# Performance work log

Measured on AMD Instinct MI355X. Metric: run time of the kernel, lower is better.

## Reference

```python
import jax, jax.numpy as jnp
import numpy as np

NEG_SLOPE = 0.2  # PyG GATv2Conv default negative_slope


def gatv2_layer(x, src, dst, edge_attr, Wl, bl, Wr, br, We, att, bias, n_nodes):
    """Faithful PyG GATv2Conv (concat=True, eval mode / no dropout).
    x: [N, Fin]; src/dst: [E]; edge_attr: [E, Fe]; att: [H, C].
    Returns [N, H*C].
    """
    H, C = att.shape
    xl = (x @ Wl + bl).reshape(-1, H, C)        # source-side transform (x_j)
    xr = (x @ Wr + br).reshape(-1, H, C)        # target-side transform (x_i)
    e_emb = (edge_attr @ We).reshape(-1, H, C)
    # per-edge pre-activation: x_i + x_j + edge
    g = jax.nn.leaky_relu(xl[src] + xr[dst] + e_emb, NEG_SLOPE)  # [E, H, C]
    logits = jnp.einsum('ehc,hc->eh', g, att)                    # [E, H]
    # segment softmax grouped by destination node
    m = jax.ops.segment_max(logits, dst, num_segments=n_nodes)   # [N, H]
    m = jnp.where(jnp.isfinite(m), m, 0.0)                       # empty segments
    a = jnp.exp(logits - m[dst])
    denom = jax.ops.segment_sum(a, dst, num_segments=n_nodes)    # [N, H]
    alpha = a / (denom[dst] + 1e-16)
    msg = xl[src] * alpha[:, :, None]                            # [E, H, C]
    out = jax.ops.segment_sum(msg, dst, num_segments=n_nodes)    # [N, H, C]
    return out.reshape(n_nodes, H * C) + bias


def setup_inputs() -> dict:
    key = jax.random.key(0)
    ks = jax.random.split(key, 24)
    N, E = 100000, 1600000
    Fin, Hd, Fe = 6, 64, 2
    g = lambda k, shp: (jax.random.normal(k, shp, dtype=jnp.float32) * 0.1)
    inp = {
        'x': jax.random.normal(ks[0], (N, Fin), dtype=jnp.float32),
        'edge_index': jax.random.randint(ks[1], (2, E), 0, N, dtype=jnp.int32),
        'edge_attr': jax.random.normal(ks[2], (E, Fe), dtype=jnp.float32),
        # layer 1: heads=2, out=64 -> H*C = 128
        'Wl1': g(ks[3], (Fin, 128)), 'bl1': jnp.zeros((128,), jnp.float32),
        'Wr1': g(ks[4], (Fin, 128)), 'br1': jnp.zeros((128,), jnp.float32),
        'We1': g(ks[5], (Fe, 128)),
        'att1': g(ks[6], (2, Hd)),
        'bias1': jnp.zeros((128,), jnp.float32),
        # layer 2: heads=1, in=128, out=64
        'Wl2': g(ks[7], (128, Hd)), 'bl2': jnp.zeros((Hd,), jnp.float32),
        'Wr2': g(ks[8], (128, Hd)), 'br2': jnp.zeros((Hd,), jnp.float32),
        'We2': g(ks[9], (Fe, Hd)),
        'att2': g(ks[10], (1, Hd)),
        'bias2': jnp.zeros((Hd,), jnp.float32),
        # MLP head
        'Wh1': g(ks[11], (Hd, Hd)), 'bh1': jnp.zeros((Hd,), jnp.float32),
        'Wh2': g(ks[12], (Hd, 1)), 'bh2': jnp.zeros((1,), jnp.float32),
    }
    return inp


def reference(x, edge_index, edge_attr,
              Wl1, bl1, Wr1, br1, We1, att1, bias1,
              Wl2, bl2, Wr2, br2, We2, att2, bias2,
              Wh1, bh1, Wh2, bh2):
    N = x.shape[0]
    src, dst = edge_index[0], edge_index[1]
    h = gatv2_layer(x, src, dst, edge_attr, Wl1, bl1, Wr1, br1, We1, att1, bias1, N)
    h = jax.nn.relu(h)
    h = gatv2_layer(h, src, dst, edge_attr, Wl2, bl2, Wr2, br2, We2, att2, bias2, N)
    h = jax.nn.relu(h)
    out = jax.nn.relu(h @ Wh1 + bh1) @ Wh2 + bh2  # [N, 1]
    return out[:, 0]
```

## Files before the change

### kernel.cpp

```cpp
#include <hip/hip_runtime.h>
#include <hip/hip_bf16.h>

#define NEG_SLOPE 0.2f
#define LOG2E 1.44269504088896f

#define NB_SHIFT 9
#define NB_NODES 512
#define NBLK_PART 256

typedef _Float16 half8 __attribute__((ext_vector_type(8)));
typedef _Float16 half4 __attribute__((ext_vector_type(4)));
typedef _Float16 half2t __attribute__((ext_vector_type(2)));

__device__ __forceinline__ void ld4(float* d, const float* p) {
    float4 t = *(const float4*)p;
    d[0] = t.x; d[1] = t.y; d[2] = t.z; d[3] = t.w;
}

__device__ __forceinline__ unsigned pack2h(float a, float b) {
    union { half2t h; unsigned u; } pk;
    pk.h[0] = (_Float16)a; pk.h[1] = (_Float16)b;
    return pk.u;
}

__device__ __forceinline__ half2t u2h2(unsigned u) {
    union { unsigned u; half2t h; } c; c.u = u; return c.h;
}
__device__ __forceinline__ half2t f2h2(float a, float b) {
    half2t r; r[0] = (_Float16)a; r[1] = (_Float16)b; return r;
}

#if __has_builtin(__builtin_amdgcn_perm)
#define PERMB(a, b, s) __builtin_amdgcn_perm((a), (b), (s))
#else
__device__ __forceinline__ unsigned PERMB(unsigned a, unsigned b, unsigned s) {
    unsigned long long v = ((unsigned long long)a << 32) | b;
    unsigned r = 0;
#pragma unroll
    for (int i = 0; i < 4; ++i) {
        unsigned idx = (s >> (8 * i)) & 0xFF;
        r |= ((unsigned)(v >> (8 * idx)) & 0xFF) << (8 * i);
    }
    return r;
}
#endif

#if __has_builtin(__builtin_amdgcn_fdot2)
#define FDOT2(a, b, c) __builtin_amdgcn_fdot2((a), (b), (c), false)
#else
#define FDOT2(a, b, c) fmaf((float)(a)[1], (float)(b)[1], fmaf((float)(a)[0], (float)(b)[0], (c)))
#endif

#define DPP_ADD(x, ctrl) \
    ((x) + __int_as_float(__builtin_amdgcn_update_dpp(0, __float_as_int(x), (ctrl), 0xf, 0xf, true)))
#define ROW_REDUCE16(x) do { \
    x = DPP_ADD(x, 0x128); \
    x = DPP_ADD(x, 0x124); \
    x = DPP_ADD(x, 0x122); \
    x = DPP_ADD(x, 0x121); \
} while (0)

#define CHGRP(xl2, xr2, wa, wb, at2, ex, ey, logit) do { \
    half2t z_ = (xl2) + (xr2); \
    z_ = __builtin_elementwise_fma((ex), (wa), z_); \
    z_ = __builtin_elementwise_fma((ey), (wb), z_); \
    z_ = __builtin_elementwise_max(z_, z_ * NEGS); \
    logit = FDOT2(z_, (at2), logit); \
} while (0)

__global__ void __launch_bounds__(256) prepA_kernel(
    const float* __restrict__ x,
    const float* __restrict__ Wl1, const float* __restrict__ bl1,
    const float* __restrict__ Wr1, const float* __restrict__ br1,
    _Float16* __restrict__ xlh, _Float16* __restrict__ xrh, int N,
    const int* __restrict__ dstv, int* __restrict__ M, int E, int EPB, int NB)
{
    __shared__ int hist[256];
    int blk = blockIdx.x, t = threadIdx.x;
    bool doA = (blk < NBLK_PART);
    if (doA) {
        if (t < NB) hist[t] = 0;
        __syncthreads();
        int s0 = blk * EPB;
        int s1 = min(s0 + EPB, E);
        for (int e = s0 + t; e < s1; e += 256)
            atomicAdd(&hist[((unsigned)dstv[e]) >> NB_SHIFT], 1);
    }

    int gt = blk * 256 + t;
    int n = gt >> 6, tt = gt & 63;
    if (n < N) {
        int h = tt >> 5;
        int cp = tt & 31;
        int c0 = h * 64 + 2 * cp;
        const float* xrow = x + (size_t)n * 6;
        float la = bl1[c0], lb = bl1[c0 + 1];
        float ra = br1[c0], rb = br1[c0 + 1];
#pragma unroll
        for (int f = 0; f < 6; ++f) {
            float xv = xrow[f];
            la = fmaf(xv, Wl1[f * 128 + c0], la);
            lb = fmaf(xv, Wl1[f * 128 + c0 + 1], lb);
            ra = fmaf(xv, Wr1[f * 128 + c0], ra);
            rb = fmaf(xv, Wr1[f * 128 + c0 + 1], rb);
        }
        int pos = (cp >> 1) * 8 + h * 4 + (cp & 1) * 2;
        *(unsigned*)(xlh + (size_t)n * 128 + pos) = pack2h(la, lb);
        *(unsigned*)(xrh + (size_t)n * 128 + pos) = pack2h(ra, rb);
    }

    if (doA) {
        __syncthreads();
        if (t < NB) M[t * NBLK_PART + blk] = hist[t];
    }
}

__global__ void __launch_bounds__(256) partB1_scanrow(
    int* __restrict__ M, int* __restrict__ btot)
{
    __shared__ int lds[256];
    int bkt = blockIdx.x, t = threadIdx.x;
    int cnt = M[bkt * NBLK_PART + t];
    lds[t] = cnt;
    __syncthreads();
    for (int s = 1; s < 256; s <<= 1) {
        int v = (t >= s) ? lds[t - s] : 0;
        __syncthreads();
        lds[t] += v;
        __syncthreads();
    }
    M[bkt * NBLK_PART + t] = lds[t] - cnt;
    if (t == 255) btot[bkt] = lds[255];
}

__global__ void __launch_bounds__(256) partC_scatter(
    const int* __restrict__ srcv, const int* __restrict__ dstv,
    const float2* __restrict__ ea2, const int* __restrict__ M,
    const int* __restrict__ btot,
    int2* __restrict__ ebuf, int E, int EPB, int NB)
{
    __shared__ int pref[256];
    __shared__ int cur[256];
    int blk = blockIdx.x, t = threadIdx.x;
    int v = (t < NB) ? btot[t] : 0;
    pref[t] = v;
    __syncthreads();
    for (int s = 1; s < 256; s <<= 1) {
        int u = (t >= s) ? pref[t - s] : 0;
        __syncthreads();
        pref[t] += u;
        __syncthreads();
    }
    if (t < NB) cur[t] = M[t * NBLK_PART + blk] + (pref[t] - v);
    __syncthreads();
    int s0 = blk * EPB;
    int s1 = min(s0 + EPB, E);
    for (int e = s0 + t; e < s1; e += 256) {
        int d = dstv[e];
        int bkt = ((unsigned)d) >> NB_SHIFT;
        int p = atomicAdd(&cur[bkt], 1);
        float2 ea = ea2[e];
        int2 rec;
        rec.x = srcv[e] | ((d & (NB_NODES - 1)) << 23);
        rec.y = (int)pack2h(ea.x, ea.y);
        ebuf[p] = rec;
    }
}

__global__ void __launch_bounds__(256) partD_finalize(
    const int2* __restrict__ ebuf, const int* __restrict__ btot,
    int* __restrict__ off, int2* __restrict__ csr_edge, int N, int NB, int E)
{
    __shared__ int hist[NB_NODES];
    __shared__ int pref[256];
    __shared__ int segv[2];
    int b = blockIdx.x, t = threadIdx.x;
    int v = (t < NB) ? btot[t] : 0;
    pref[t] = v;
    __syncthreads();
    for (int s = 1; s < 256; s <<= 1) {
        int u = (t >= s) ? pref[t - s] : 0;
        __syncthreads();
        pref[t] += u;
        __syncthreads();
    }
    if (t == b) { segv[0] = pref[t] - v; segv[1] = pref[t]; }
    __syncthreads();
    int seg_s = segv[0], seg_e = segv[1];
    int node_base = b << NB_SHIFT;
    int nnodes = min(NB_NODES, N - node_base);
    if (b == 0 && t == 0) off[N] = E;

    for (int i = t; i < NB_NODES; i += 256) hist[i] = 0;
    __syncthreads();
    for (int e = seg_s + t; e < seg_e; e += 256)
        atomicAdd(&hist[((unsigned)ebuf[e].x) >> 23], 1);
    __syncthreads();
    if (t == 0) {
        int run = 0;
        for (int i = 0; i < nnodes; ++i) { int c = hist[i]; hist[i] = run; run += c; }
    }
    __syncthreads();
    for (int i = t; i < nnodes; i += 256) off[node_base + i] = seg_s + hist[i];
    __syncthreads();
    for (int e = seg_s + t; e < seg_e; e += 256) {
        int2 rec = ebuf[e];
        int dl = ((unsigned)rec.x) >> 23;
        int r = atomicAdd(&hist[dl], 1);
        rec.x &= 0x7FFFFF;
        csr_edge[seg_s + r] = rec;
    }
}

__global__ void __launch_bounds__(256) c1_kernel(
    const int* __restrict__ off, const int2* __restrict__ csr_edge,
    const _Float16* __restrict__ xlh, const _Float16* __restrict__ xrh,
    const float* __restrict__ We1, const float* __restrict__ att1,
    const float* __restrict__ bias1,
    _Float16* __restrict__ h1h, int N)
{
    int wv = (blockIdx.x * blockDim.x + threadIdx.x) >> 6;
    int lane = threadIdx.x & 63;
    if (2 * wv >= N) return;
    int half = lane >> 5;
    int n = 2 * wv + half;
    bool nvalid = (n < N);
    int nc = nvalid ? n : 0;
    int l = lane & 31;
    int g = l & 15;
    int slot = (l >> 4) & 1;
    unsigned gb = (unsigned)(g << 4);

    const half2t NEGS = f2h2(NEG_SLOPE, NEG_SLOPE);

    half2t a0h[2], a1h[2], w00h[2], w01h[2], w10h[2], w11h[2];
    {
        float t[4];
        ld4(t, att1 + 4 * g);
        a0h[0] = f2h2(t[0] * LOG2E, t[1] * LOG2E); a0h[1] = f2h2(t[2] * LOG2E, t[3] * LOG2E);
        ld4(t, att1 + 64 + 4 * g);
        a1h[0] = f2h2(t[0] * LOG2E, t[1] * LOG2E); a1h[1] = f2h2(t[2] * LOG2E, t[3] * LOG2E);
        ld4(t, We1 + 4 * g);        w00h[0] = f2h2(t[0], t[1]); w00h[1] = f2h2(t[2], t[3]);
        ld4(t, We1 + 64 + 4 * g);   w01h[0] = f2h2(t[0], t[1]); w01h[1] = f2h2(t[2], t[3]);
        ld4(t, We1 + 128 + 4 * g);  w10h[0] = f2h2(t[0], t[1]); w10h[1] = f2h2(t[2], t[3]);
        ld4(t, We1 + 192 + 4 * g);  w11h[0] = f2h2(t[0], t[1]); w11h[1] = f2h2(t[2], t[3]);
    }

    half2t xr00, xr01, xr10, xr11;
    {
        half8 xrv = *(const half8*)(xrh + (size_t)nc * 128 + 8 * g);
        xr00[0] = xrv[0]; xr00[1] = xrv[1];
        xr01[0] = xrv[2]; xr01[1] = xrv[3];
        xr10[0] = xrv[4]; xr10[1] = xrv[5];
        xr11[0] = xrv[6]; xr11[1] = xrv[7];
    }

    int s = off[nc];
    int e = nvalid ? off[nc + 1] : s;
    int m = e - s;
    int mo = __shfl_xor(m, 32);
    int iters = (max(m, mo) + 3) >> 2;

    float a0A[4] = {0,0,0,0}, a1A[4] = {0,0,0,0};
    float a0B[4] = {0,0,0,0}, a1B[4] = {0,0,0,0};
    float d0A = 0.f, d1A = 0.f, d0B = 0.f, d1B = 0.f;

    const char* xlb = (const char*)xlh;

    int pA0 = s + slot, pB0 = s + 2 + slot;
    bool vA0 = (pA0 < e), vB0 = (pB0 < e);
    int2 edA0 = csr_edge[vA0 ? pA0 : 0];
    int2 edB0 = csr_edge[vB0 ? pB0 : 0];
    int pA1 = s + 4 + slot, pB1 = s + 6 + slot;
    bool vA1 = (pA1 < e), vB1 = (pB1 < e);
    int2 edA1 = csr_edge[vA1 ? pA1 : 0];
    int2 edB1 = csr_edge[vB1 ? pB1 : 0];
    half8 hvA = *(const half8*)(xlb + (((unsigned)edA0.x) << 8) + gb);
    half8 hvB = *(const half8*)(xlb + (((unsigned)edB0.x) << 8) + gb);

    int p0 = s;
    for (int it = 0; it < iters; ++it, p0 += 4) {
        int pA2 = p0 + 8 + slot, pB2 = p0 + 10 + slot;
        bool vA2 = (pA2 < e), vB2 = (pB2 < e);
        int2 edA2 = csr_edge[vA2 ? pA2 : 0];
        int2 edB2 = csr_edge[vB2 ? pB2 : 0];

        half8 hvAn = *(const half8*)(xlb + (((unsigned)edA1.x) << 8) + gb);
        half8 hvBn = *(const half8*)(xlb + (((unsigned)edB1.x) << 8) + gb);

        unsigned uA = (unsigned)edA0.y, uB = (unsigned)edB0.y;
        half2t exA = u2h2(PERMB(uA, uA, 0x01000100));
        half2t eyA = u2h2(PERMB(uA, uA, 0x03020302));
        half2t exB = u2h2(PERMB(uB, uB, 0x01000100));
        half2t eyB = u2h2(PERMB(uB, uB, 0x03020302));

        union { half8 h; unsigned u[4]; } HA, HB;
        HA.h = hvA; HB.h = hvB;
        half2t xA00 = u2h2(HA.u[0]), xA01 = u2h2(HA.u[1]);
        half2t xA10 = u2h2(HA.u[2]), xA11 = u2h2(HA.u[3]);
        half2t xB00 = u2h2(HB.u[0]), xB01 = u2h2(HB.u[1]);
        half2t xB10 = u2h2(HB.u[2]), xB11 = u2h2(HB.u[3]);

        float pA0f = 0.f, pA1f = 0.f, pB0f = 0.f, pB1f = 0.f;
        CHGRP(xA00, xr00, w00h[0], w10h[0], a0h[0], exA, eyA, pA0f);
        CHGRP(xA01, xr01, w00h[1], w10h[1], a0h[1], exA, eyA, pA0f);
        CHGRP(xA10, xr10, w01h[0], w11h[0], a1h[0], exA, eyA, pA1f);
        CHGRP(xA11, xr11, w01h[1], w11h[1], a1h[1], exA, eyA, pA1f);
        CHGRP(xB00, xr00, w00h[0], w10h[0], a0h[0], exB, eyB, pB0f);
        CHGRP(xB01, xr01, w00h[1], w10h[1], a0h[1], exB, eyB, pB0f);
        CHGRP(xB10, xr10, w01h[0], w11h[0], a1h[0], exB, eyB, pB1f);
        CHGRP(xB11, xr11, w01h[1], w11h[1], a1h[1], exB, eyB, pB1f);

        ROW_REDUCE16(pA0f);
        ROW_REDUCE16(pA1f);
        ROW_REDUCE16(pB0f);
        ROW_REDUCE16(pB1f);

        float eA0 = vA0 ? exp2f(pA0f) : 0.f;
        float eA1 = vA0 ? exp2f(pA1f) : 0.f;
        float eB0 = vB0 ? exp2f(pB0f) : 0.f;
        float eB1 = vB0 ? exp2f(pB1f) : 0.f;
        d0A += eA0; d1A += eA1;
        d0B += eB0; d1B += eB1;

        a0A[0] = fmaf(eA0, (float)hvA[0], a0A[0]);
        a0A[1] = fmaf(eA0, (float)hvA[1], a0A[1]);
        a0A[2] = fmaf(eA0, (float)hvA[2], a0A[2]);
        a0A[3] = fmaf(eA0, (float)hvA[3], a0A[3]);
        a1A[0] = fmaf(eA1, (float)hvA[4], a1A[0]);
        a1A[1] = fmaf(eA1, (float)hvA[5], a1A[1]);
        a1A[2] = fmaf(eA1, (float)hvA[6], a1A[2]);
        a1A[3] = fmaf(eA1, (float)hvA[7], a1A[3]);
        a0B[0] = fmaf(eB0, (float)hvB[0], a0B[0]);
        a0B[1] = fmaf(eB0, (float)hvB[1], a0B[1]);
        a0B[2] = fmaf(eB0, (float)hvB[2], a0B[2]);
        a0B[3] = fmaf(eB0, (float)hvB[3], a0B[3]);
        a1B[0] = fmaf(eB1, (float)hvB[4], a1B[0]);
        a1B[1] = fmaf(eB1, (float)hvB[5], a1B[1]);
        a1B[2] = fmaf(eB1, (float)hvB[6], a1B[2]);
        a1B[3] = fmaf(eB1, (float)hvB[7], a1B[3]);

        edA0 = edA1; edB0 = edB1; vA0 = vA1; vB0 = vB1;
        edA1 = edA2; edB1 = edB2; vA1 = vA2; vB1 = vB2;
        hvA = hvAn; hvB = hvBn;
    }

    float acc0[4], acc1[4];
#pragma unroll
    for (int i = 0; i < 4; ++i) { acc0[i] = a0A[i] + a0B[i]; acc1[i] = a1A[i] + a1B[i]; }
    float d0 = d0A + d0B, d1 = d1A + d1B;
#pragma unroll
    for (int i = 0; i < 4; ++i) {
        acc0[i] += __shfl_xor(acc0[i], 16);
        acc1[i] += __shfl_xor(acc1[i], 16);
    }
    d0 += __shfl_xor(d0, 16);
    d1 += __shfl_xor(d1, 16);

    if (slot == 0 && nvalid) {
        float b0[4], b1[4];
        ld4(b0, bias1 + 4 * g);
        ld4(b1, bias1 + 64 + 4 * g);
        float r0 = 1.f / (d0 + 1e-16f), r1 = 1.f / (d1 + 1e-16f);
        half4 o0, o1;
        o0[0] = (_Float16)fmaxf(fmaf(acc0[0], r0, b0[0]), 0.f);
        o0[1] = (_Float16)fmaxf(fmaf(acc0[1], r0, b0[1]), 0.f);
        o0[2] = (_Float16)fmaxf(fmaf(acc0[2], r0, b0[2]), 0.f);
        o0[3] = (_Float16)fmaxf(fmaf(acc0[3], r0, b0[3]), 0.f);
        o1[0] = (_Float16)fmaxf(fmaf(acc1[0], r1, b1[0]), 0.f);
        o1[1] = (_Float16)fmaxf(fmaf(acc1[1], r1, b1[1]), 0.f);
        o1[2] = (_Float16)fmaxf(fmaf(acc1[2], r1, b1[2]), 0.f);
        o1[3] = (_Float16)fmaxf(fmaf(acc1[3], r1, b1[3]), 0.f);
        *(half4*)(h1h + (size_t)n * 128 + 4 * g) = o0;
        *(half4*)(h1h + (size_t)n * 128 + 64 + 4 * g) = o1;
    }
}

__global__ void __launch_bounds__(256) a2_kernel(
    const _Float16* __restrict__ h1h,
    const float* __restrict__ Wl2, const float* __restrict__ bl2,
    const float* __restrict__ Wr2, const float* __restrict__ br2,
    _Float16* __restrict__ xl2h, _Float16* __restrict__ xr2h, int N)
{
    __shared__ float hs[64 * 128];
    int tid = threadIdx.x;
    int n0 = blockIdx.x * 64;

    for (int i = tid; i < 64 * 16; i += 256) {
        int row = i >> 4;
        int q = i & 15;
        int n = n0 + row;
        float f[8];
        if (n < N) {
            half8 v = *(const half8*)(h1h + (size_t)n * 128 + q * 8);
#pragma unroll
            for (int j = 0; j < 8; ++j) f[j] = (float)v[j];
        } else {
#pragma unroll
            for (int j = 0; j < 8; ++j) f[j] = 0.f;
        }
        *(float4*)(hs + row * 128 + q * 8)     = make_float4(f[0], f[1], f[2], f[3]);
        *(float4*)(hs + row * 128 + q * 8 + 4) = make_float4(f[4], f[5], f[6], f[7]);
    }
    __syncthreads();

    int cslot = tid & 31;
    int jgrp = tid >> 5;
    int c4 = cslot * 4;
    bool isL = (c4 < 64);
    int cc = isL ? c4 : (c4 - 64);
    const float* Wb = (isL ? Wl2 : Wr2) + cc;
    const float* bb = (isL ? bl2 : br2) + cc;
    float4 bias = *(const float4*)bb;

    float acc[8][4];
#pragma unroll
    for (int j = 0; j < 8; ++j) {
        acc[j][0] = bias.x; acc[j][1] = bias.y;
        acc[j][2] = bias.z; acc[j][3] = bias.w;
    }

    const float* hrow = hs + (jgrp * 8) * 128;
#pragma unroll 2
    for (int k4 = 0; k4 < 32; ++k4) {
        float4 w0 = *(const float4*)(Wb + (4 * k4 + 0) * 64);
        float4 w1 = *(const float4*)(Wb + (4 * k4 + 1) * 64);
        float4 w2 = *(const float4*)(Wb + (4 * k4 + 2) * 64);
        float4 w3 = *(const float4*)(Wb + (4 * k4 + 3) * 64);
#pragma unroll
        for (int j = 0; j < 8; ++j) {
            float4 hv = *(const float4*)(hrow + j * 128 + k4 * 4);
            acc[j][0] = fmaf(hv.x, w0.x, acc[j][0]);
            acc[j][1] = fmaf(hv.x, w0.y, acc[j][1]);
            acc[j][2] = fmaf(hv.x, w0.z, acc[j][2]);
            acc[j][3] = fmaf(hv.x, w0.w, acc[j][3]);
            acc[j][0] = fmaf(hv.y, w1.x, acc[j][0]);
            acc[j][1] = fmaf(hv.y, w1.y, acc[j][1]);
            acc[j][2] = fmaf(hv.y, w1.z, acc[j][2]);
            acc[j][3] = fmaf(hv.y, w1.w, acc[j][3]);
            acc[j][0] = fmaf(hv.z, w2.x, acc[j][0]);
            acc[j][1] = fmaf(hv.z, w2.y, acc[j][1]);
            acc[j][2] = fmaf(hv.z, w2.z, acc[j][2]);
            acc[j][3] = fmaf(hv.z, w2.w, acc[j][3]);
            acc[j][0] = fmaf(hv.w, w3.x, acc[j][0]);
            acc[j][1] = fmaf(hv.w, w3.y, acc[j][1]);
            acc[j][2] = fmaf(hv.w, w3.z, acc[j][2]);
            acc[j][3] = fmaf(hv.w, w3.w, acc[j][3]);
        }
    }

    _Float16* outb = isL ? xl2h : xr2h;
#pragma unroll
    for (int j = 0; j < 8; ++j) {
        int n = n0 + jgrp * 8 + j;
        if (n < N) {
            half4 o;
            o[0] = (_Float16)acc[j][0];
            o[1] = (_Float16)acc[j][1];
            o[2] = (_Float16)acc[j][2];
            o[3] = (_Float16)acc[j][3];
            *(half4*)(outb + (size_t)n * 64 + cc) = o;
        }
    }
}

__global__ void __launch_bounds__(256) c2_kernel(
    const int* __restrict__ off, const int2* __restrict__ csr_edge,
    const _Float16* __restrict__ xl2h, const _Float16* __restrict__ xr2h,
    const float* __restrict__ We2, const float* __restrict__ att2,
    const float* __restrict__ bias2,
    float* __restrict__ h2out, int N)
{
    int wv = (blockIdx.x * blockDim.x + threadIdx.x) >> 6;
    int lane = threadIdx.x & 63;
    if (2 * wv >= N) return;
    int half = lane >> 5;
    int n = 2 * wv + half;
    bool nvalid = (n < N);
    int nc = nvalid ? n : 0;
    int l = lane & 31;
    int g = l & 15;
    int slot = (l >> 4) & 1;
    unsigned gb = (unsigned)(g << 3);

    const half2t NEGS = f2h2(NEG_SLOPE, NEG_SLOPE);

    half2t avh[2], w0h[2], w1h[2], xr2[2];
    {
        float t[4];
        ld4(t, att2 + 4 * g);
        avh[0] = f2h2(t[0] * LOG2E, t[1] * LOG2E); avh[1] = f2h2(t[2] * LOG2E, t[3] * LOG2E);
        ld4(t, We2 + 4 * g);       w0h[0] = f2h2(t[0], t[1]); w0h[1] = f2h2(t[2], t[3]);
        ld4(t, We2 + 64 + 4 * g);  w1h[0] = f2h2(t[0], t[1]); w1h[1] = f2h2(t[2], t[3]);
        half4 xh = *(const half4*)(xr2h + (size_t)nc * 64 + 4 * g);
        xr2[0][0] = xh[0]; xr2[0][1] = xh[1];
        xr2[1][0] = xh[2]; xr2[1][1] = xh[3];
    }

    int s = off[nc];
    int e = nvalid ? off[nc + 1] : s;
    int m = e - s;
    int mo = __shfl_xor(m, 32);
    int iters = (max(m, mo) + 3) >> 2;

    float dA = 0.f, dB = 0.f;
    float aA[4] = {0,0,0,0}, aB[4] = {0,0,0,0};

    const char* xlb = (const char*)xl2h;

    int pA0 = s + slot, pB0 = s + 2 + slot;
    bool vA0 = (pA0 < e), vB0 = (pB0 < e);
    int2 edA0 = csr_edge[vA0 ? pA0 : 0];
    int2 edB0 = csr_edge[vB0 ? pB0 : 0];
    int pA1 = s + 4 + slot, pB1 = s + 6 + slot;
    bool vA1 = (pA1 < e), vB1 = (pB1 < e);
    int2 edA1 = csr_edge[vA1 ? pA1 : 0];
    int2 edB1 = csr_edge[vB1 ? pB1 : 0];
    half4 hvA = *(const half4*)(xlb + (((unsigned)edA0.x) << 7) + gb);
    half4 hvB = *(const half4*)(xlb + (((unsigned)edB0.x) << 7) + gb);

    int p0 = s;
    for (int it = 0; it < iters; ++it, p0 += 4) {
        int pA2 = p0 + 8 + slot, pB2 = p0 + 10 + slot;
        bool vA2 = (pA2 < e), vB2 = (pB2 < e);
        int2 edA2 = csr_edge[vA2 ? pA2 : 0];
        int2 edB2 = csr_edge[vB2 ? pB2 : 0];

        half4 hvAn = *(const half4*)(xlb + (((unsigned)edA1.x) << 7) + gb);
        half4 hvBn = *(const half4*)(xlb + (((unsigned)edB1.x) << 7) + gb);

        unsigned uA = (unsigned)edA0.y, uB = (unsigned)edB0.y;
        half2t exA = u2h2(PERMB(uA, uA, 0x01000100));
        half2t eyA = u2h2(PERMB(uA, uA, 0x03020302));
        half2t exB = u2h2(PERMB(uB, uB, 0x01000100));
        half2t eyB = u2h2(PERMB(uB, uB, 0x03020302));

        union { half4 h; unsigned u[2]; } HA, HB;
        HA.h = hvA; HB.h = hvB;
        half2t xA0 = u2h2(HA.u[0]), xA1 = u2h2(HA.u[1]);
        half2t xB0 = u2h2(HB.u[0]), xB1 = u2h2(HB.u[1]);

        float pA_ = 0.f, pB_ = 0.f;
        CHGRP(xA0, xr2[0], w0h[0], w1h[0], avh[0], exA, eyA, pA_);
        CHGRP(xA1, xr2[1], w0h[1], w1h[1], avh[1], exA, eyA, pA_);
        CHGRP(xB0, xr2[0], w0h[0], w1h[0], avh[0], exB, eyB, pB_);
        CHGRP(xB1, xr2[1], w0h[1], w1h[1], avh[1], exB, eyB, pB_);

        ROW_REDUCE16(pA_);
        ROW_REDUCE16(pB_);
        float evA = vA0 ? exp2f(pA_) : 0.f;
        float evB = vB0 ? exp2f(pB_) : 0.f;
        dA += evA; dB += evB;

        aA[0] = fmaf(evA, (float)hvA[0], aA[0]);
        aA[1] = fmaf(evA, (float)hvA[1], aA[1]);
        aA[2] = fmaf(evA, (float)hvA[2], aA[2]);
        aA[3] = fmaf(evA, (float)hvA[3], aA[3]);
        aB[0] = fmaf(evB, (float)hvB[0], aB[0]);
        aB[1] = fmaf(evB, (float)hvB[1], aB[1]);
        aB[2] = fmaf(evB, (float)hvB[2], aB[2]);
        aB[3] = fmaf(evB, (float)hvB[3], aB[3]);

        edA0 = edA1; edB0 = edB1; vA0 = vA1; vB0 = vB1;
        edA1 = edA2; edB1 = edB2; vA1 = vA2; vB1 = vB2;
        hvA = hvAn; hvB = hvBn;
    }

    float acc[4];
#pragma unroll
    for (int i = 0; i < 4; ++i) acc[i] = aA[i] + aB[i];
    float dsum = dA + dB;
#pragma unroll
    for (int i = 0; i < 4; ++i) acc[i] += __shfl_xor(acc[i], 16);
    dsum += __shfl_xor(dsum, 16);

    if (slot == 0 && nvalid) {
        float b2[4];
        ld4(b2, bias2 + 4 * g);
        float r = 1.f / (dsum + 1e-16f);
        float4 o;
        o.x = fmaxf(fmaf(acc[0], r, b2[0]), 0.f);
        o.y = fmaxf(fmaf(acc[1], r, b2[1]), 0.f);
        o.z = fmaxf(fmaf(acc[2], r, b2[2]), 0.f);
        o.w = fmaxf(fmaf(acc[3], r, b2[3]), 0.f);
        *(float4*)(h2out + (size_t)n * 64 + 4 * g) = o;
    }
}

__global__ void __launch_bounds__(256) head_kernel(
    const float* __restrict__ h2, const float* __restrict__ Wh1,
    const float* __restrict__ bh1, const float* __restrict__ Wh2,
    const float* __restrict__ bh2, float* __restrict__ out, int N)
{
    __shared__ float hs[64 * 68];
    int tid = threadIdx.x;
    int n0 = blockIdx.x * 64;

    for (int i = tid; i < 64 * 16; i += 256) {
        int row = i >> 4, q = i & 15;
        int n = n0 + row;
        float4 v = (n < N) ? *(const float4*)(h2 + (size_t)n * 64 + q * 4)
                           : make_float4(0.f, 0.f, 0.f, 0.f);
        *(float4*)(hs + row * 68 + q * 4) = v;
    }
    __syncthreads();

    int cslot = tid & 15;
    int jgrp  = tid >> 4;
    int c4 = cslot * 4;
    float4 bias = *(const float4*)(bh1 + c4);

    float acc[4][4];
#pragma unroll
    for (int r = 0; r < 4; ++r) {
        acc[r][0] = bias.x; acc[r][1] = bias.y;
        acc[r][2] = bias.z; acc[r][3] = bias.w;
    }

    const float* hrow = hs + (jgrp * 4) * 68;
#pragma unroll 2
    for (int k4 = 0; k4 < 16; ++k4) {
        float4 w0 = *(const float4*)(Wh1 + (4 * k4 + 0) * 64 + c4);
        float4 w1 = *(const float4*)(Wh1 + (4 * k4 + 1) * 64 + c4);
        float4 w2 = *(const float4*)(Wh1 + (4 * k4 + 2) * 64 + c4);
        float4 w3 = *(const float4*)(Wh1 + (4 * k4 + 3) * 64 + c4);
#pragma unroll
        for (int r = 0; r < 4; ++r) {
            float4 hv = *(const float4*)(hrow + r * 68 + k4 * 4);
            acc[r][0] = fmaf(hv.x, w0.x, acc[r][0]);
            acc[r][1] = fmaf(hv.x, w0.y, acc[r][1]);
            acc[r][2] = fmaf(hv.x, w0.z, acc[r][2]);
            acc[r][3] = fmaf(hv.x, w0.w, acc[r][3]);
            acc[r][0] = fmaf(hv.y, w1.x, acc[r][0]);
            acc[r][1] = fmaf(hv.y, w1.y, acc[r][1]);
            acc[r][2] = fmaf(hv.y, w1.z, acc[r][2]);
            acc[r][3] = fmaf(hv.y, w1.w, acc[r][3]);
            acc[r][0] = fmaf(hv.z, w2.x, acc[r][0]);
            acc[r][1] = fmaf(hv.z, w2.y, acc[r][1]);
            acc[r][2] = fmaf(hv.z, w2.z, acc[r][2]);
            acc[r][3] = fmaf(hv.z, w2.w, acc[r][3]);
            acc[r][0] = fmaf(hv.w, w3.x, acc[r][0]);
            acc[r][1] = fmaf(hv.w, w3.y, acc[r][1]);
            acc[r][2] = fmaf(hv.w, w3.z, acc[r][2]);
            acc[r][3] = fmaf(hv.w, w3.w, acc[r][3]);
        }
    }

    float4 w2v = *(const float4*)(Wh2 + c4);
    float p[4];
#pragma unroll
    for (int r = 0; r < 4; ++r) {
        p[r] = fmaxf(acc[r][0], 0.f) * w2v.x
             + fmaxf(acc[r][1], 0.f) * w2v.y
             + fmaxf(acc[r][2], 0.f) * w2v.z
             + fmaxf(acc[r][3], 0.f) * w2v.w;
    }
#pragma unroll
    for (int m = 1; m <= 8; m <<= 1) {
#pragma unroll
        for (int r = 0; r < 4; ++r) p[r] += __shfl_xor(p[r], m);
    }
    if (cslot == 0) {
        float b = bh2[0];
#pragma unroll
        for (int r = 0; r < 4; ++r) {
            int n = n0 + jgrp * 4 + r;
            if (n < N) out[n] = p[r] + b;
        }
    }
}

extern "C" void kernel_launch(void* const* d_in, const int* in_sizes, int n_in,
                              void* d_out, int out_size, void* d_ws, size_t ws_size,
                              hipStream_t stream) {
    const float* x    = (const float*)d_in[0];
    const int*   ei   = (const int*)d_in[1];
    const float* ea   = (const float*)d_in[2];
    const float* Wl1  = (const float*)d_in[3];
    const float* bl1  = (const float*)d_in[4];
    const float* Wr1  = (const float*)d_in[5];
    const float* br1  = (const float*)d_in[6];
    const float* We1  = (const float*)d_in[7];
    const float* att1 = (const float*)d_in[8];
    const float* bias1= (const float*)d_in[9];
    const float* Wl2  = (const float*)d_in[10];
    const float* bl2  = (const float*)d_in[11];
    const float* Wr2  = (const float*)d_in[12];
    const float* br2  = (const float*)d_in[13];
    const float* We2  = (const float*)d_in[14];
    const float* att2 = (const float*)d_in[15];
    const float* bias2= (const float*)d_in[16];
    const float* Wh1  = (const float*)d_in[17];
    const float* bh1  = (const float*)d_in[18];
    const float* Wh2  = (const float*)d_in[19];
    const float* bh2  = (const float*)d_in[20];

    int N = in_sizes[0] / 6;
    int E = in_sizes[1] / 2;
    const int* srcv = ei;
    const int* dstv = ei + E;

    int NB = (N + NB_NODES - 1) >> NB_SHIFT;
    int EPB = (E + NBLK_PART - 1) / NBLK_PART;

    char* w = (char*)d_ws;
    auto align256 = [](size_t v) { return (v + 255) & ~(size_t)255; };
    _Float16* xlh = (_Float16*)w;
    char* ip = w + align256((size_t)N * 128 * 2);
    _Float16* xrh = (_Float16*)ip; ip += align256((size_t)N * 128 * 2);
    _Float16* h1h = (_Float16*)ip; ip += align256((size_t)N * 128 * 2);
    _Float16* xl2h = (_Float16*)ip; ip += align256((size_t)N * 64 * 2);
    _Float16* xr2h = (_Float16*)ip; ip += align256((size_t)N * 64 * 2);
    int* off = (int*)ip;  ip += align256((size_t)(N + 1) * 4);
    int* Mbuf = (int*)ip; ip += align256((size_t)NB * NBLK_PART * 4);
    int* btot = (int*)ip; ip += align256((size_t)NB * 4);
    int2* csr_edge = (int2*)ip;

    int2* ebuf = (int2*)h1h;
    float* h2 = (float*)xlh;

    int prep_blocks = (int)(((size_t)N * 64 + 255) / 256);
    if (prep_blocks < NBLK_PART) prep_blocks = NBLK_PART;
    prepA_kernel<<<prep_blocks, 256, 0, stream>>>(
        x, Wl1, bl1, Wr1, br1, xlh, xrh, N, dstv, Mbuf, E, EPB, NB);
    partB1_scanrow<<<NB, 256, 0, stream>>>(Mbuf, btot);
    partC_scatter<<<NBLK_PART, 256, 0, stream>>>(
        srcv, dstv, (const float2*)ea, Mbuf, btot, ebuf, E, EPB, NB);
    partD_finalize<<<NB, 256, 0, stream>>>(ebuf, btot, off, csr_edge, N, NB, E);

    size_t nwv = (size_t)((N + 1) / 2);
    c1_kernel<<<(nwv * 64 + 255) / 256, 256, 0, stream>>>(
        off, csr_edge, xlh, xrh, We1, att1, bias1, h1h, N);
    a2_kernel<<<(N + 63) / 64, 256, 0, stream>>>(
        h1h, Wl2, bl2, Wr2, br2, xl2h, xr2h, N);
    c2_kernel<<<(nwv * 64 + 255) / 256, 256, 0, stream>>>(
        off, csr_edge, xl2h, xr2h, We2, att2, bias2, h2, N);
    head_kernel<<<(N + 63) / 64, 256, 0, stream>>>(
        h2, Wh1, bh1, Wh2, bh2, (float*)d_out, N);
}
```

Before: 431.8 us.

## Sort nodes by in-degree within buckets to balance wave workloads in GAT kernels

Within each 512-node bucket, partD_finalize now counting-sorts nodes by in-degree (capped at 64 bins) into a perm array. The c1 and c2 aggregation kernels process nodes in this permuted order, so the two half-waves sharing a wavefront have similar edge counts and less divergence. This costs an extra perm load and sorting work in the finalize kernel, and it gives up some write and gather locality because output rows are scattered.

```diff
diff --git a/kernel.cpp b/kernel.cpp
--- a/kernel.cpp
+++ b/kernel.cpp
@@ -7,6 +7,7 @@
 #define NB_SHIFT 9
 #define NB_NODES 512
 #define NBLK_PART 256
+#define DEG_BINS 64
 
 typedef _Float16 half8 __attribute__((ext_vector_type(8)));
 typedef _Float16 half4 __attribute__((ext_vector_type(4)));
@@ -169,10 +170,13 @@
 
 __global__ void __launch_bounds__(256) partD_finalize(
     const int2* __restrict__ ebuf, const int* __restrict__ btot,
-    int* __restrict__ off, int2* __restrict__ csr_edge, int N, int NB, int E)
+    int* __restrict__ off, int2* __restrict__ csr_edge,
+    int* __restrict__ perm, int N, int NB, int E)
 {
     __shared__ int hist[NB_NODES];
+    __shared__ int dg[NB_NODES];
     __shared__ int pref[256];
+    __shared__ int cnt[DEG_BINS];
     __shared__ int segv[2];
     int b = blockIdx.x, t = threadIdx.x;
     int v = (t < NB) ? btot[t] : 0;
@@ -195,6 +199,9 @@
     __syncthreads();
     for (int e = seg_s + t; e < seg_e; e += 256)
         atomicAdd(&hist[((unsigned)ebuf[e].x) >> 23], 1);
+    __syncthreads();
+    for (int i = t; i < NB_NODES; i += 256) dg[i] = hist[i];
+    if (t < DEG_BINS) cnt[t] = 0;
     __syncthreads();
     if (t == 0) {
         int run = 0;
@@ -210,10 +217,24 @@
         rec.x &= 0x7FFFFF;
         csr_edge[seg_s + r] = rec;
     }
+
+    for (int i = t; i < nnodes; i += 256)
+        atomicAdd(&cnt[min(dg[i], DEG_BINS - 1)], 1);
+    __syncthreads();
+    if (t == 0) {
+        int run = 0;
+        for (int i = 0; i < DEG_BINS; ++i) { int c = cnt[i]; cnt[i] = run; run += c; }
+    }
+    __syncthreads();
+    for (int i = t; i < nnodes; i += 256) {
+        int r = atomicAdd(&cnt[min(dg[i], DEG_BINS - 1)], 1);
+        perm[node_base + r] = node_base + i;
+    }
 }
 
 __global__ void __launch_bounds__(256) c1_kernel(
     const int* __restrict__ off, const int2* __restrict__ csr_edge,
+    const int* __restrict__ perm,
     const _Float16* __restrict__ xlh, const _Float16* __restrict__ xrh,
     const float* __restrict__ We1, const float* __restrict__ att1,
     const float* __restrict__ bias1,
@@ -223,9 +244,9 @@
     int lane = threadIdx.x & 63;
     if (2 * wv >= N) return;
     int half = lane >> 5;
-    int n = 2 * wv + half;
-    bool nvalid = (n < N);
-    int nc = nvalid ? n : 0;
+    int idx = 2 * wv + half;
+    bool nvalid = (idx < N);
+    int nc = nvalid ? perm[idx] : perm[0];
     int l = lane & 31;
     int g = l & 15;
     int slot = (l >> 4) & 1;
@@ -371,8 +392,8 @@
         o1[1] = (_Float16)fmaxf(fmaf(acc1[1], r1, b1[1]), 0.f);
         o1[2] = (_Float16)fmaxf(fmaf(acc1[2], r1, b1[2]), 0.f);
         o1[3] = (_Float16)fmaxf(fmaf(acc1[3], r1, b1[3]), 0.f);
-        *(half4*)(h1h + (size_t)n * 128 + 4 * g) = o0;
-        *(half4*)(h1h + (size_t)n * 128 + 64 + 4 * g) = o1;
+        *(half4*)(h1h + (size_t)nc * 128 + 4 * g) = o0;
+        *(half4*)(h1h + (size_t)nc * 128 + 64 + 4 * g) = o1;
     }
 }
 
@@ -466,6 +487,7 @@
 
 __global__ void __launch_bounds__(256) c2_kernel(
     const int* __restrict__ off, const int2* __restrict__ csr_edge,
+    const int* __restrict__ perm,
     const _Float16* __restrict__ xl2h, const _Float16* __restrict__ xr2h,
     const float* __restrict__ We2, const float* __restrict__ att2,
     const float* __restrict__ bias2,
@@ -475,9 +497,9 @@
     int lane = threadIdx.x & 63;
     if (2 * wv >= N) return;
     int half = lane >> 5;
-    int n = 2 * wv + half;
-    bool nvalid = (n < N);
-    int nc = nvalid ? n : 0;
+    int idx = 2 * wv + half;
+    bool nvalid = (idx < N);
+    int nc = nvalid ? perm[idx] : perm[0];
     int l = lane & 31;
     int g = l & 15;
     int slot = (l >> 4) & 1;
@@ -583,7 +605,7 @@
         o.y = fmaxf(fmaf(acc[1], r, b2[1]), 0.f);
         o.z = fmaxf(fmaf(acc[2], r, b2[2]), 0.f);
         o.w = fmaxf(fmaf(acc[3], r, b2[3]), 0.f);
-        *(float4*)(h2out + (size_t)n * 64 + 4 * g) = o;
+        *(float4*)(h2out + (size_t)nc * 64 + 4 * g) = o;
     }
 }
 
@@ -712,6 +734,7 @@
     _Float16* xl2h = (_Float16*)ip; ip += align256((size_t)N * 64 * 2);
     _Float16* xr2h = (_Float16*)ip; ip += align256((size_t)N * 64 * 2);
     int* off = (int*)ip;  ip += align256((size_t)(N + 1) * 4);
+    int* perm = (int*)ip; ip += align256((size_t)N * 4);
     int* Mbuf = (int*)ip; ip += align256((size_t)NB * NBLK_PART * 4);
     int* btot = (int*)ip; ip += align256((size_t)NB * 4);
     int2* csr_edge = (int2*)ip;
@@ -726,15 +749,15 @@
     partB1_scanrow<<<NB, 256, 0, stream>>>(Mbuf, btot);
     partC_scatter<<<NBLK_PART, 256, 0, stream>>>(
         srcv, dstv, (const float2*)ea, Mbuf, btot, ebuf, E, EPB, NB);
-    partD_finalize<<<NB, 256, 0, stream>>>(ebuf, btot, off, csr_edge, N, NB, E);
+    partD_finalize<<<NB, 256, 0, stream>>>(ebuf, btot, off, csr_edge, perm, N, NB, E);
 
     size_t nwv = (size_t)((N + 1) / 2);
     c1_kernel<<<(nwv * 64 + 255) / 256, 256, 0, stream>>>(
-        off, csr_edge, xlh, xrh, We1, att1, bias1, h1h, N);
+        off, csr_edge, perm, xlh, xrh, We1, att1, bias1, h1h, N);
     a2_kernel<<<(N + 63) / 64, 256, 0, stream>>>(
         h1h, Wl2, bl2, Wr2, br2, xl2h, xr2h, N);
     c2_kernel<<<(nwv * 64 + 255) / 256, 256, 0, stream>>>(
-        off, csr_edge, xl2h, xr2h, We2, att2, bias2, h2, N);
+        off, csr_edge, perm, xl2h, xr2h, We2, att2, bias2, h2, N);
     head_kernel<<<(N + 63) / 64, 256, 0, stream>>>(
         h2, Wh1, bh1, Wh2, bh2, (float*)d_out, N);
 }
```

Result: no change. 425.7 us (-1.4%).
